# Optimization experiments

Measured on AMD Instinct MI355X. Metric: run time of the kernel, lower is better.

## Reference

```python
import jax, jax.numpy as jnp
import numpy as np
from jax.ops import segment_sum

NUM_HEADS = 16
NEG_INF = -jnp.inf


def setup_inputs() -> dict:
    key = jax.random.key(0)
    ks = jax.random.split(key, 12)
    D, H = 1024, NUM_HEADS
    SRC, TGT = 2048, 2048
    V, EV = 32000, 2000
    s = 1.0 / np.sqrt(D)
    return {
        "logits": jax.random.normal(ks[0], (TGT, V), jnp.float32),
        "extended_vocab_ids": jax.random.randint(ks[1], (SRC,), 0, V + EV, jnp.int32),
        "src_subtokens": jax.random.normal(ks[2], (SRC, D), jnp.float32),
        "tgt_subtokens": jax.random.normal(ks[3], (TGT, D), jnp.float32),
        "w_q": jax.random.normal(ks[4], (D, D), jnp.float32) * s,
        "b_q": jax.random.normal(ks[5], (D,), jnp.float32) * 0.02,
        "w_k": jax.random.normal(ks[6], (D, D), jnp.float32) * s,
        "b_k": jax.random.normal(ks[7], (D,), jnp.float32) * 0.02,
        "w_ptr": jax.random.normal(ks[8], (D,), jnp.float32) * s,
        "b_ptr": jax.random.normal(ks[9], (1,), jnp.float32) * 0.02,
        "len_vocab": V,
        "len_extended_vocab": EV,
    }


def _mha_attention(query, key, w_q, b_q, w_k, b_k):
    # SimpleMHA.unbatched_forward: project q/k, per-head scaled dot-product
    # softmax over src, mean over heads -> [TGT, SRC]
    TGT, D = query.shape
    SRC = key.shape[0]
    hd = D // NUM_HEADS
    q = (query @ w_q.T + b_q).reshape(TGT, NUM_HEADS, hd)
    k = (key @ w_k.T + b_k).reshape(SRC, NUM_HEADS, hd)
    scores = jnp.einsum("thd,shd->hts", q, k) / jnp.sqrt(jnp.float32(hd))
    attn = jax.nn.softmax(scores, axis=-1)  # [H, TGT, SRC]
    return attn.mean(axis=0)  # [TGT, SRC]


def reference(logits, extended_vocab_ids, src_subtokens, tgt_subtokens,
              w_q, b_q, w_k, b_k, w_ptr, b_ptr, len_vocab, len_extended_vocab):
    total = len_vocab + len_extended_vocab
    eps = jnp.finfo(jnp.float32).eps
    fmin = jnp.finfo(jnp.float32).min

    # copy gate: sigmoid(Linear(tgt)) -> [TGT, 1]
    copy_prob = jax.nn.sigmoid(tgt_subtokens @ w_ptr + b_ptr[0])[:, None]

    # attention distribution over src tokens [TGT, SRC]
    attn = _mha_attention(tgt_subtokens, src_subtokens, w_q, b_q, w_k, b_k)

    # attention @ one-hot(M) == scatter-add of attention columns by vocab id
    attn_vocab = segment_sum(attn.T, extended_vocab_ids, num_segments=total).T  # [TGT, total]
    attn_vocab = jnp.where(attn_vocab == 0, eps, attn_vocab)
    pointer_log_probs = jnp.log(attn_vocab)

    decoder_log_probs = jax.nn.log_softmax(logits, axis=1)
    decoder_log_probs = jnp.pad(decoder_log_probs, ((0, 0), (0, len_extended_vocab)),
                                constant_values=NEG_INF)

    p = jnp.stack([decoder_log_probs + jnp.log(1.0 - copy_prob),
                   pointer_log_probs + jnp.log(copy_prob)])
    p = jnp.where(p == NEG_INF, fmin, p)
    return jax.scipy.special.logsumexp(p, axis=0)
```

## Files before the change

### kernel.cpp

```cpp
#include <hip/hip_runtime.h>

typedef __attribute__((ext_vector_type(8))) short short8;
typedef __attribute__((ext_vector_type(4))) float f32x4;
typedef __attribute__((ext_vector_type(4))) unsigned int u32x4;
typedef unsigned short u16;
typedef unsigned int u32;

#define MFMA16 __builtin_amdgcn_mfma_f32_16x16x32_bf16

static constexpr int TGT = 2048, SRCN = 2048, DIM = 1024, NH = 16;
static constexpr int NV = 32000, NTOT = 34000;
#define FLT_EPS 1.1920928955078125e-07f

__device__ __forceinline__ u16 f2bf(float f) {
  unsigned u = __float_as_uint(f);
  return (u16)((u + 0x7FFFu + ((u >> 16) & 1u)) >> 16);
}

__device__ __forceinline__ int swz8(int row, int seg) {
  return row * 64 + ((seg ^ (row & 7)) << 3);
}

__global__ __launch_bounds__(256) void proj_gemm(
    const float* __restrict__ Xq, const float* __restrict__ Wq,
    const float* __restrict__ Bq, u16* __restrict__ Cq,
    const float* __restrict__ Xk, const float* __restrict__ Wk,
    const float* __restrict__ Bk, u16* __restrict__ Ck) {
  const int zz = blockIdx.z;
  const float* X = zz ? Xk : Xq;
  const float* W = zz ? Wk : Wq;
  const float* bias = zz ? Bk : Bq;
  u16* C = zz ? Ck : Cq;
  const float scale = zz ? 1.0f : 0.125f;

  __shared__ u16 As[128 * 32];
  __shared__ u16 Bs[128 * 32];
  const int n0 = blockIdx.x * 128, m0 = blockIdx.y * 128;
  const int tid = threadIdx.x, lane = tid & 63, w = tid >> 6;
  const int wr = w >> 1, wc = w & 1;
  const int srow = tid >> 1, shalf = tid & 1;
  f32x4 acc[4][4] = {};

  for (int k0 = 0; k0 < DIM; k0 += 32) {
    __syncthreads();
    {
      const float* pa = X + (size_t)(m0 + srow) * DIM + k0 + shalf * 16;
      const float* pb = W + (size_t)(n0 + srow) * DIM + k0 + shalf * 16;
      float4 a0 = ((const float4*)pa)[0], a1 = ((const float4*)pa)[1];
      float4 a2 = ((const float4*)pa)[2], a3 = ((const float4*)pa)[3];
      float4 b0 = ((const float4*)pb)[0], b1 = ((const float4*)pb)[1];
      float4 b2 = ((const float4*)pb)[2], b3 = ((const float4*)pb)[3];
      short8 wa0, wa1, wb0, wb1;
      wa0[0]=(short)f2bf(a0.x); wa0[1]=(short)f2bf(a0.y); wa0[2]=(short)f2bf(a0.z); wa0[3]=(short)f2bf(a0.w);
      wa0[4]=(short)f2bf(a1.x); wa0[5]=(short)f2bf(a1.y); wa0[6]=(short)f2bf(a1.z); wa0[7]=(short)f2bf(a1.w);
      wa1[0]=(short)f2bf(a2.x); wa1[1]=(short)f2bf(a2.y); wa1[2]=(short)f2bf(a2.z); wa1[3]=(short)f2bf(a2.w);
      wa1[4]=(short)f2bf(a3.x); wa1[5]=(short)f2bf(a3.y); wa1[6]=(short)f2bf(a3.z); wa1[7]=(short)f2bf(a3.w);
      wb0[0]=(short)f2bf(b0.x); wb0[1]=(short)f2bf(b0.y); wb0[2]=(short)f2bf(b0.z); wb0[3]=(short)f2bf(b0.w);
      wb0[4]=(short)f2bf(b1.x); wb0[5]=(short)f2bf(b1.y); wb0[6]=(short)f2bf(b1.z); wb0[7]=(short)f2bf(b1.w);
      wb1[0]=(short)f2bf(b2.x); wb1[1]=(short)f2bf(b2.y); wb1[2]=(short)f2bf(b2.z); wb1[3]=(short)f2bf(b2.w);
      wb1[4]=(short)f2bf(b3.x); wb1[5]=(short)f2bf(b3.y); wb1[6]=(short)f2bf(b3.z); wb1[7]=(short)f2bf(b3.w);
      int swz = (srow >> 1) & 3;
      int sg0 = ((shalf * 2 + 0) ^ swz) << 3;
      int sg1 = ((shalf * 2 + 1) ^ swz) << 3;
      *(short8*)&As[srow * 32 + sg0] = wa0;
      *(short8*)&As[srow * 32 + sg1] = wa1;
      *(short8*)&Bs[srow * 32 + sg0] = wb0;
      *(short8*)&Bs[srow * 32 + sg1] = wb1;
    }
    __syncthreads();
    const int kq = lane >> 4;
    short8 af[4], bfr[4];
    for (int f = 0; f < 4; ++f) {
      int ar = wr * 64 + f * 16 + (lane & 15);
      af[f] = *(const short8*)&As[ar * 32 + ((kq ^ ((ar >> 1) & 3)) << 3)];
      int br = wc * 64 + f * 16 + (lane & 15);
      bfr[f] = *(const short8*)&Bs[br * 32 + ((kq ^ ((br >> 1) & 3)) << 3)];
    }
    for (int fr = 0; fr < 4; ++fr)
      for (int fc = 0; fc < 4; ++fc)
        acc[fr][fc] = MFMA16(af[fr], bfr[fc], acc[fr][fc], 0, 0, 0);
  }

  for (int fc = 0; fc < 4; ++fc) {
    int col = n0 + wc * 64 + fc * 16 + (lane & 15);
    float bv = bias[col];
    for (int fr = 0; fr < 4; ++fr)
      for (int r = 0; r < 4; ++r) {
        int rowm = m0 + wr * 64 + fr * 16 + ((lane >> 4) << 2) + r;
        C[(size_t)rowm * DIM + col] = f2bf((acc[fr][fc][r] + bv) * scale);
      }
  }
}

__global__ __launch_bounds__(256) void zsum_kernel(const u16* __restrict__ Qb,
                                                   const u16* __restrict__ Kb,
                                                   float* __restrict__ Zinv) {
  __shared__ u16 Ks[64 * 64];
  const int h = blockIdx.x, t0 = blockIdx.y * 64;
  const int tid = threadIdx.x, lane = tid & 63, w = tid >> 6;
  const int arow = t0 + w * 16 + (lane & 15);
  const int acol = h * 64 + ((lane >> 4) << 3);
  short8 a0 = *(const short8*)&Qb[(size_t)arow * DIM + acol];
  short8 a1 = *(const short8*)&Qb[(size_t)arow * DIM + acol + 32];
  float zacc[4] = {0.f, 0.f, 0.f, 0.f};

  for (int s0 = 0; s0 < SRCN; s0 += 64) {
    __syncthreads();
    for (int q = tid; q < 512; q += 256) {
      int r = q >> 3, seg = q & 7;
      *(short8*)&Ks[swz8(r, seg)] = *(const short8*)&Kb[(size_t)(s0 + r) * DIM + h * 64 + seg * 8];
    }
    __syncthreads();
    for (int sub = 0; sub < 4; ++sub) {
      int brow = sub * 16 + (lane & 15);
      int slo = (lane >> 4);
      short8 b0 = *(const short8*)&Ks[swz8(brow, slo)];
      short8 b1 = *(const short8*)&Ks[swz8(brow, slo + 4)];
      f32x4 c = {0.f, 0.f, 0.f, 0.f};
      c = MFMA16(a0, b0, c, 0, 0, 0);
      c = MFMA16(a1, b1, c, 0, 0, 0);
      zacc[0] += __expf(c[0]); zacc[1] += __expf(c[1]);
      zacc[2] += __expf(c[2]); zacc[3] += __expf(c[3]);
    }
  }
  for (int d = 1; d < 16; d <<= 1) {
    zacc[0] += __shfl_xor(zacc[0], d, 64);
    zacc[1] += __shfl_xor(zacc[1], d, 64);
    zacc[2] += __shfl_xor(zacc[2], d, 64);
    zacc[3] += __shfl_xor(zacc[3], d, 64);
  }
  if ((lane & 15) == 0) {
    int trow = t0 + w * 16 + ((lane >> 4) << 2);
    for (int r = 0; r < 4; ++r)
      Zinv[h * TGT + trow + r] = 1.0f / (16.0f * zacc[r]);
  }
}

__global__ __launch_bounds__(256) void fused_mid_kernel(
    const u16* __restrict__ Qb, const u16* __restrict__ Kb,
    const float* __restrict__ Zinv, float* __restrict__ attn,
    const float* __restrict__ logits, const float* __restrict__ tgt,
    const float* __restrict__ w_ptr, const float* __restrict__ b_ptr,
    const int* __restrict__ ids, int* __restrict__ sperm,
    u32* __restrict__ segmap, float4* __restrict__ rowc) {
  __shared__ __align__(16) char smem[20480];
  const int b = blockIdx.x;
  const int tid = threadIdx.x, lane = tid & 63, w = tid >> 6;

  if (b == 0) {
    int* kk_ = (int*)smem;
    int* vv_ = (int*)(smem + 8192);
    for (int i = tid; i < 2048; i += 256) { kk_[i] = ids[i]; vv_[i] = i; }
    __syncthreads();
    for (int kk = 2; kk <= 2048; kk <<= 1)
      for (int j = kk >> 1; j > 0; j >>= 1) {
        for (int m = tid; m < 1024; m += 256) {
          int i = ((m & ~(j - 1)) << 1) | (m & (j - 1));
          int l = i | j;
          bool asc = ((i & kk) == 0);
          int ki = kk_[i], kl = kk_[l];
          if ((ki > kl) == asc) {
            kk_[i] = kl; kk_[l] = ki;
            int tv = vv_[i]; vv_[i] = vv_[l]; vv_[l] = tv;
          }
        }
        __syncthreads();
      }
    for (int i = tid; i < 2048; i += 256) sperm[i] = vv_[i];
    for (int i = tid; i < NTOT; i += 256) segmap[i] = 0xFFFFFFFFu;
    __syncthreads();
    for (int p = tid; p < 2048; p += 256) {
      int id = kk_[p];
      if (p > 0 && kk_[p - 1] == id) continue;
      int q = p + 1;
      while (q < 2048 && kk_[q] == id) ++q;
      segmap[id] = (u32)p | ((u32)(q - p) << 16);
    }
    return;
  }

  if (b <= 1024) {
    u16* Qs = (u16*)smem;
    u16* Ks = (u16*)(smem + 8192);
    float* izs = (float*)(smem + 16384);
    const int bb = b - 1;
    const int s0 = (bb & 31) * 64, t0 = (bb >> 5) * 64;
    const int wr = w >> 1, wc = w & 1;
    for (int q = tid; q < 1024; q += 256) izs[q] = Zinv[(q >> 6) * TGT + t0 + (q & 63)];
    f32x4 acc[2][2] = {};

    for (int h = 0; h < NH; ++h) {
      __syncthreads();
      for (int q = tid; q < 512; q += 256) {
        int r = q >> 3, seg = q & 7;
        *(short8*)&Qs[swz8(r, seg)] = *(const short8*)&Qb[(size_t)(t0 + r) * DIM + h * 64 + seg * 8];
        *(short8*)&Ks[swz8(r, seg)] = *(const short8*)&Kb[(size_t)(s0 + r) * DIM + h * 64 + seg * 8];
      }
      __syncthreads();
      f32x4 sc[2][2] = {};
      for (int kk = 0; kk < 2; ++kk) {
        int seg = (lane >> 4) + kk * 4;
        short8 a0 = *(const short8*)&Qs[swz8(wr * 32 + (lane & 15), seg)];
        short8 a1 = *(const short8*)&Qs[swz8(wr * 32 + 16 + (lane & 15), seg)];
        short8 b0 = *(const short8*)&Ks[swz8(wc * 32 + (lane & 15), seg)];
        short8 b1 = *(const short8*)&Ks[swz8(wc * 32 + 16 + (lane & 15), seg)];
        sc[0][0] = MFMA16(a0, b0, sc[0][0], 0, 0, 0);
        sc[0][1] = MFMA16(a0, b1, sc[0][1], 0, 0, 0);
        sc[1][0] = MFMA16(a1, b0, sc[1][0], 0, 0, 0);
        sc[1][1] = MFMA16(a1, b1, sc[1][1], 0, 0, 0);
      }
      for (int fr = 0; fr < 2; ++fr)
        for (int fc = 0; fc < 2; ++fc)
          for (int r = 0; r < 4; ++r) {
            float iz = izs[h * 64 + wr * 32 + fr * 16 + ((lane >> 4) << 2) + r];
            acc[fr][fc][r] += __expf(sc[fr][fc][r]) * iz;
          }
    }
    for (int fr = 0; fr < 2; ++fr)
      for (int fc = 0; fc < 2; ++fc)
        for (int r = 0; r < 4; ++r) {
          int t = t0 + wr * 32 + fr * 16 + ((lane >> 4) << 2) + r;
          int s = s0 + wc * 32 + fc * 16 + (lane & 15);
          attn[(size_t)t * SRCN + s] = acc[fr][fc][r];
        }
    return;
  }

  float* red = (float*)smem;
  const int t = b - 1025;
  const f32x4* l4 = (const f32x4*)(logits + (size_t)t * NV);
  float e0 = 0.f, e1 = 0.f, e2 = 0.f, e3 = 0.f;
  const f32x4 z4 = {0.f, 0.f, 0.f, 0.f};
#pragma unroll 2
  for (int pk = 0; pk < 8; ++pk) {
    int g0 = pk * 1024 + tid;
    int g1 = g0 + 256, g2 = g0 + 512, g3 = g0 + 768;
    bool d0 = g0 < NV / 4, d1 = g1 < NV / 4, d2 = g2 < NV / 4, d3 = g3 < NV / 4;
    f32x4 v0 = d0 ? l4[g0] : z4;
    f32x4 v1 = d1 ? l4[g1] : z4;
    f32x4 v2 = d2 ? l4[g2] : z4;
    f32x4 v3 = d3 ? l4[g3] : z4;
    float s0 = (__expf(v0.x) + __expf(v0.y)) + (__expf(v0.z) + __expf(v0.w));
    float s1 = (__expf(v1.x) + __expf(v1.y)) + (__expf(v1.z) + __expf(v1.w));
    float s2 = (__expf(v2.x) + __expf(v2.y)) + (__expf(v2.z) + __expf(v2.w));
    float s3 = (__expf(v3.x) + __expf(v3.y)) + (__expf(v3.z) + __expf(v3.w));
    e0 += d0 ? s0 : 0.f;
    e1 += d1 ? s1 : 0.f;
    e2 += d2 ? s2 : 0.f;
    e3 += d3 ? s3 : 0.f;
  }
  float es = (e0 + e1) + (e2 + e3);

  float4 xv = *(const float4*)&tgt[(size_t)t * DIM + tid * 4];
  float4 wv = *(const float4*)&w_ptr[tid * 4];
  float g = (xv.x * wv.x + xv.y * wv.y) + (xv.z * wv.z + xv.w * wv.w);
  for (int d = 1; d < 64; d <<= 1) {
    es += __shfl_xor(es, d, 64);
    g += __shfl_xor(g, d, 64);
  }
  if (lane == 0) { red[w] = es; red[4 + w] = g; }
  __syncthreads();
  if (tid == 0) {
    float tot = red[0] + red[1] + red[2] + red[3];
    float gs = red[4] + red[5] + red[6] + red[7] + b_ptr[0];
    float c = 1.0f / (1.0f + __expf(-gs));
    float4 rc;
    rc.x = (1.0f - c) / tot;
    rc.y = c * FLT_EPS;
    rc.z = c;
    rc.w = 0.f;
    rowc[t] = rc;
  }
}

__global__ __launch_bounds__(512) void out_kernel(
    const float* __restrict__ logits, const float4* __restrict__ rowc,
    const int* __restrict__ sperm, const u32* __restrict__ segmap,
    const float* __restrict__ attn, float* __restrict__ out) {
  const int t = blockIdx.x;
  const int tid = threadIdx.x;
  float4 rc = rowc[t];
  const float K1 = rc.x, Ceps = rc.y, cc = rc.z;
  const f32x4* l4 = (const f32x4*)(logits + (size_t)t * NV);
  const float* arow = attn + (size_t)t * SRCN;
  f32x4* o4 = (f32x4*)(out + (size_t)t * NTOT);
  const u32x4* m4 = (const u32x4*)segmap;

  auto psum = [&](u32 mv) -> float {
    if (mv == 0xFFFFFFFFu) return Ceps;
    int p = (int)(mv & 0xFFFFu), n = (int)(mv >> 16);
    float s = 0.f;
    for (int q = 0; q < n; ++q) s += arow[sperm[p + q]];
    return cc * s;
  };
  auto elem = [&](float v, bool d, u32 mv) -> float {
    float e = d ? __expf(v) : 0.f;
    return __logf(fmaf(e, K1, psum(mv)));
  };

  const f32x4 z4 = {0.f, 0.f, 0.f, 0.f};
#pragma unroll
  for (int pk = 0; pk < 4; ++pk) {
    int g0 = pk * 2048 + tid;
    int g1 = g0 + 512, g2 = g0 + 1024, g3 = g0 + 1536;
    u32x4 m0 = m4[g0], m1 = m4[g1], m2 = m4[g2], m3 = m4[g3];
    bool d0 = g0 < NV / 4, d1 = g1 < NV / 4, d2 = g2 < NV / 4, d3 = g3 < NV / 4;
    f32x4 v0 = d0 ? __builtin_nontemporal_load(&l4[g0]) : z4;
    f32x4 v1 = d1 ? __builtin_nontemporal_load(&l4[g1]) : z4;
    f32x4 v2 = d2 ? __builtin_nontemporal_load(&l4[g2]) : z4;
    f32x4 v3 = d3 ? __builtin_nontemporal_load(&l4[g3]) : z4;
    f32x4 o0, o1, o2, o3;
    o0.x = elem(v0.x, d0, m0.x); o0.y = elem(v0.y, d0, m0.y);
    o0.z = elem(v0.z, d0, m0.z); o0.w = elem(v0.w, d0, m0.w);
    o1.x = elem(v1.x, d1, m1.x); o1.y = elem(v1.y, d1, m1.y);
    o1.z = elem(v1.z, d1, m1.z); o1.w = elem(v1.w, d1, m1.w);
    o2.x = elem(v2.x, d2, m2.x); o2.y = elem(v2.y, d2, m2.y);
    o2.z = elem(v2.z, d2, m2.z); o2.w = elem(v2.w, d2, m2.w);
    o3.x = elem(v3.x, d3, m3.x); o3.y = elem(v3.y, d3, m3.y);
    o3.z = elem(v3.z, d3, m3.z); o3.w = elem(v3.w, d3, m3.w);
    __builtin_nontemporal_store(o0, &o4[g0]);
    __builtin_nontemporal_store(o1, &o4[g1]);
    __builtin_nontemporal_store(o2, &o4[g2]);
    __builtin_nontemporal_store(o3, &o4[g3]);
  }
  for (int g = 8192 + tid; g < NTOT / 4; g += 512) {
    u32x4 m = m4[g];
    f32x4 o;
    o.x = __logf(psum(m.x));
    o.y = __logf(psum(m.y));
    o.z = __logf(psum(m.z));
    o.w = __logf(psum(m.w));
    __builtin_nontemporal_store(o, &o4[g]);
  }
}

extern "C" void kernel_launch(void* const* d_in, const int* in_sizes, int n_in,
                              void* d_out, int out_size, void* d_ws, size_t ws_size,
                              hipStream_t stream) {
  const float* logits = (const float*)d_in[0];
  const int* ids      = (const int*)d_in[1];
  const float* src    = (const float*)d_in[2];
  const float* tgt    = (const float*)d_in[3];
  const float* w_q    = (const float*)d_in[4];
  const float* b_q    = (const float*)d_in[5];
  const float* w_k    = (const float*)d_in[6];
  const float* b_k    = (const float*)d_in[7];
  const float* w_ptr  = (const float*)d_in[8];
  const float* b_ptr  = (const float*)d_in[9];
  float* out = (float*)d_out;

  char* ws = (char*)d_ws;
  u16* Qb     = (u16*)(ws);
  u16* Kb     = (u16*)(ws + (size_t)4 * 1024 * 1024);
  float* Zinv = (float*)(ws + (size_t)8 * 1024 * 1024);
  float* attn = (float*)(ws + (size_t)8 * 1024 * 1024 + 131072);
  char* tail  = ws + (size_t)8 * 1024 * 1024 + 131072 + (size_t)16 * 1024 * 1024;
  int* sperm  = (int*)(tail);
  u32* segmap = (u32*)(tail + 8192);
  float4* rowc = (float4*)(tail + 8192 + 136000);

  proj_gemm<<<dim3(8, 16, 2), 256, 0, stream>>>(tgt, w_q, b_q, Qb, src, w_k, b_k, Kb);
  zsum_kernel<<<dim3(16, 32), 256, 0, stream>>>(Qb, Kb, Zinv);
  fused_mid_kernel<<<3073, 256, 0, stream>>>(Qb, Kb, Zinv, attn, logits, tgt,
                                             w_ptr, b_ptr, ids, sperm, segmap, rowc);
  out_kernel<<<TGT, 512, 0, stream>>>(logits, rowc, sperm, segmap, attn, out);
}
```

Measured before the change: 275.0 us.

## Rebalance independent row-stats and sort work across zsum and attention kernels

The independent work (logit softmax denominators, copy gate, id sort) is split across the two middle kernels. Half the row stats and the sort now run alongside the Z-sum kernel, the rest alongside the attention-column kernel, so the small zsum launch no longer underfills the GPU. The attention kernel also reads Zinv straight from global memory as float4 instead of staging it in shared memory. This balances load between launches, at the cost of more block-level branching.

Result: slower. 297.9 us (+8.4%).

```diff
diff --git a/kernel.cpp b/kernel.cpp
--- a/kernel.cpp
+++ b/kernel.cpp
@@ -19,6 +19,88 @@
 
 __device__ __forceinline__ int swz8(int row, int seg) {
   return row * 64 + ((seg ^ (row & 7)) << 3);
+}
+
+__device__ __forceinline__ void stats_row_body(
+    int t, const float* __restrict__ logits, const float* __restrict__ tgt,
+    const float* __restrict__ w_ptr, const float* __restrict__ b_ptr,
+    float4* __restrict__ rowc, int tid, int lane, int w, float* red) {
+  const f32x4* l4 = (const f32x4*)(logits + (size_t)t * NV);
+  float e0 = 0.f, e1 = 0.f, e2 = 0.f, e3 = 0.f;
+  const f32x4 z4 = {0.f, 0.f, 0.f, 0.f};
+#pragma unroll 2
+  for (int pk = 0; pk < 8; ++pk) {
+    int g0 = pk * 1024 + tid;
+    int g1 = g0 + 256, g2 = g0 + 512, g3 = g0 + 768;
+    bool d0 = g0 < NV / 4, d1 = g1 < NV / 4, d2 = g2 < NV / 4, d3 = g3 < NV / 4;
+    f32x4 v0 = d0 ? l4[g0] : z4;
+    f32x4 v1 = d1 ? l4[g1] : z4;
+    f32x4 v2 = d2 ? l4[g2] : z4;
+    f32x4 v3 = d3 ? l4[g3] : z4;
+    float s0 = (__expf(v0.x) + __expf(v0.y)) + (__expf(v0.z) + __expf(v0.w));
+    float s1 = (__expf(v1.x) + __expf(v1.y)) + (__expf(v1.z) + __expf(v1.w));
+    float s2 = (__expf(v2.x) + __expf(v2.y)) + (__expf(v2.z) + __expf(v2.w));
+    float s3 = (__expf(v3.x) + __expf(v3.y)) + (__expf(v3.z) + __expf(v3.w));
+    e0 += d0 ? s0 : 0.f;
+    e1 += d1 ? s1 : 0.f;
+    e2 += d2 ? s2 : 0.f;
+    e3 += d3 ? s3 : 0.f;
+  }
+  float es = (e0 + e1) + (e2 + e3);
+
+  float4 xv = *(const float4*)&tgt[(size_t)t * DIM + tid * 4];
+  float4 wv = *(const float4*)&w_ptr[tid * 4];
+  float g = (xv.x * wv.x + xv.y * wv.y) + (xv.z * wv.z + xv.w * wv.w);
+  for (int d = 1; d < 64; d <<= 1) {
+    es += __shfl_xor(es, d, 64);
+    g += __shfl_xor(g, d, 64);
+  }
+  if (lane == 0) { red[w] = es; red[4 + w] = g; }
+  __syncthreads();
+  if (tid == 0) {
+    float tot = red[0] + red[1] + red[2] + red[3];
+    float gs = red[4] + red[5] + red[6] + red[7] + b_ptr[0];
+    float c = 1.0f / (1.0f + __expf(-gs));
+    float4 rc;
+    rc.x = (1.0f - c) / tot;
+    rc.y = c * FLT_EPS;
+    rc.z = c;
+    rc.w = 0.f;
+    rowc[t] = rc;
+  }
+}
+
+__device__ __forceinline__ void sort_body(
+    const int* __restrict__ ids, int* __restrict__ sperm,
+    u32* __restrict__ segmap, int tid, char* smem) {
+  int* kk_ = (int*)smem;
+  int* vv_ = (int*)(smem + 8192);
+  for (int i = tid; i < 2048; i += 256) { kk_[i] = ids[i]; vv_[i] = i; }
+  __syncthreads();
+  for (int kk = 2; kk <= 2048; kk <<= 1)
+    for (int j = kk >> 1; j > 0; j >>= 1) {
+      for (int m = tid; m < 1024; m += 256) {
+        int i = ((m & ~(j - 1)) << 1) | (m & (j - 1));
+        int l = i | j;
+        bool asc = ((i & kk) == 0);
+        int ki = kk_[i], kl = kk_[l];
+        if ((ki > kl) == asc) {
+          kk_[i] = kl; kk_[l] = ki;
+          int tv = vv_[i]; vv_[i] = vv_[l]; vv_[l] = tv;
+        }
+      }
+      __syncthreads();
+    }
+  for (int i = tid; i < 2048; i += 256) sperm[i] = vv_[i];
+  for (int i = tid; i < NTOT; i += 256) segmap[i] = 0xFFFFFFFFu;
+  __syncthreads();
+  for (int p = tid; p < 2048; p += 256) {
+    int id = kk_[p];
+    if (p > 0 && kk_[p - 1] == id) continue;
+    int q = p + 1;
+    while (q < 2048 && kk_[q] == id) ++q;
+    segmap[id] = (u32)p | ((u32)(q - p) << 16);
+  }
 }
 
 __global__ __launch_bounds__(256) void proj_gemm(
@@ -92,185 +174,124 @@
   }
 }
 
-__global__ __launch_bounds__(256) void zsum_kernel(const u16* __restrict__ Qb,
-                                                   const u16* __restrict__ Kb,
-                                                   float* __restrict__ Zinv) {
-  __shared__ u16 Ks[64 * 64];
-  const int h = blockIdx.x, t0 = blockIdx.y * 64;
+__global__ __launch_bounds__(256) void fused_a_kernel(
+    const u16* __restrict__ Qb, const u16* __restrict__ Kb,
+    float* __restrict__ Zinv,
+    const float* __restrict__ logits, const float* __restrict__ tgt,
+    const float* __restrict__ w_ptr, const float* __restrict__ b_ptr,
+    const int* __restrict__ ids, int* __restrict__ sperm,
+    u32* __restrict__ segmap, float4* __restrict__ rowc) {
+  __shared__ __align__(16) char smem[16384];
+  const int b = blockIdx.x;
   const int tid = threadIdx.x, lane = tid & 63, w = tid >> 6;
-  const int arow = t0 + w * 16 + (lane & 15);
-  const int acol = h * 64 + ((lane >> 4) << 3);
-  short8 a0 = *(const short8*)&Qb[(size_t)arow * DIM + acol];
-  short8 a1 = *(const short8*)&Qb[(size_t)arow * DIM + acol + 32];
-  float zacc[4] = {0.f, 0.f, 0.f, 0.f};
-
-  for (int s0 = 0; s0 < SRCN; s0 += 64) {
-    __syncthreads();
-    for (int q = tid; q < 512; q += 256) {
-      int r = q >> 3, seg = q & 7;
-      *(short8*)&Ks[swz8(r, seg)] = *(const short8*)&Kb[(size_t)(s0 + r) * DIM + h * 64 + seg * 8];
-    }
-    __syncthreads();
-    for (int sub = 0; sub < 4; ++sub) {
-      int brow = sub * 16 + (lane & 15);
-      int slo = (lane >> 4);
-      short8 b0 = *(const short8*)&Ks[swz8(brow, slo)];
-      short8 b1 = *(const short8*)&Ks[swz8(brow, slo + 4)];
-      f32x4 c = {0.f, 0.f, 0.f, 0.f};
-      c = MFMA16(a0, b0, c, 0, 0, 0);
-      c = MFMA16(a1, b1, c, 0, 0, 0);
-      zacc[0] += __expf(c[0]); zacc[1] += __expf(c[1]);
-      zacc[2] += __expf(c[2]); zacc[3] += __expf(c[3]);
-    }
-  }
-  for (int d = 1; d < 16; d <<= 1) {
-    zacc[0] += __shfl_xor(zacc[0], d, 64);
-    zacc[1] += __shfl_xor(zacc[1], d, 64);
-    zacc[2] += __shfl_xor(zacc[2], d, 64);
-    zacc[3] += __shfl_xor(zacc[3], d, 64);
-  }
-  if ((lane & 15) == 0) {
-    int trow = t0 + w * 16 + ((lane >> 4) << 2);
-    for (int r = 0; r < 4; ++r)
-      Zinv[h * TGT + trow + r] = 1.0f / (16.0f * zacc[r]);
-  }
-}
-
-__global__ __launch_bounds__(256) void fused_mid_kernel(
+
+  if (b < 1024) {
+    stats_row_body(b, logits, tgt, w_ptr, b_ptr, rowc, tid, lane, w, (float*)smem);
+    return;
+  }
+  if (b == 1536) {
+    sort_body(ids, sperm, segmap, tid, smem);
+    return;
+  }
+  {
+    u16* Ks = (u16*)smem;
+    const int bb = b - 1024;
+    const int h = bb & 15, t0 = (bb >> 4) * 64;
+    const int arow = t0 + w * 16 + (lane & 15);
+    const int acol = h * 64 + ((lane >> 4) << 3);
+    short8 a0 = *(const short8*)&Qb[(size_t)arow * DIM + acol];
+    short8 a1 = *(const short8*)&Qb[(size_t)arow * DIM + acol + 32];
+    float zacc[4] = {0.f, 0.f, 0.f, 0.f};
+
+    for (int s0 = 0; s0 < SRCN; s0 += 64) {
+      __syncthreads();
+      for (int q = tid; q < 512; q += 256) {
+        int r = q >> 3, seg = q & 7;
+        *(short8*)&Ks[swz8(r, seg)] = *(const short8*)&Kb[(size_t)(s0 + r) * DIM + h * 64 + seg * 8];
+      }
+      __syncthreads();
+      for (int sub = 0; sub < 4; ++sub) {
+        int brow = sub * 16 + (lane & 15);
+        int slo = (lane >> 4);
+        short8 b0 = *(const short8*)&Ks[swz8(brow, slo)];
+        short8 b1 = *(const short8*)&Ks[swz8(brow, slo + 4)];
+        f32x4 c = {0.f, 0.f, 0.f, 0.f};
+        c = MFMA16(a0, b0, c, 0, 0, 0);
+        c = MFMA16(a1, b1, c, 0, 0, 0);
+        zacc[0] += __expf(c[0]); zacc[1] += __expf(c[1]);
+        zacc[2] += __expf(c[2]); zacc[3] += __expf(c[3]);
+      }
+    }
+    for (int d = 1; d < 16; d <<= 1) {
+      zacc[0] += __shfl_xor(zacc[0], d, 64);
+      zacc[1] += __shfl_xor(zacc[1], d, 64);
+      zacc[2] += __shfl_xor(zacc[2], d, 64);
+      zacc[3] += __shfl_xor(zacc[3], d, 64);
+    }
+    if ((lane & 15) == 0) {
+      int trow = t0 + w * 16 + ((lane >> 4) << 2);
+      for (int r = 0; r < 4; ++r)
+        Zinv[h * TGT + trow + r] = 1.0f / (16.0f * zacc[r]);
+    }
+  }
+}
+
+__global__ __launch_bounds__(256) void fused_b_kernel(
     const u16* __restrict__ Qb, const u16* __restrict__ Kb,
     const float* __restrict__ Zinv, float* __restrict__ attn,
     const float* __restrict__ logits, const float* __restrict__ tgt,
     const float* __restrict__ w_ptr, const float* __restrict__ b_ptr,
-    const int* __restrict__ ids, int* __restrict__ sperm,
-    u32* __restrict__ segmap, float4* __restrict__ rowc) {
-  __shared__ __align__(16) char smem[20480];
+    float4* __restrict__ rowc) {
+  __shared__ __align__(16) char smem[16384];
   const int b = blockIdx.x;
   const int tid = threadIdx.x, lane = tid & 63, w = tid >> 6;
 
-  if (b == 0) {
-    int* kk_ = (int*)smem;
-    int* vv_ = (int*)(smem + 8192);
-    for (int i = tid; i < 2048; i += 256) { kk_[i] = ids[i]; vv_[i] = i; }
+  if (b >= 1024) {
+    stats_row_body(b, logits, tgt, w_ptr, b_ptr, rowc, tid, lane, w, (float*)smem);
+    return;
+  }
+  u16* Qs = (u16*)smem;
+  u16* Ks = (u16*)(smem + 8192);
+  const int s0 = (b & 31) * 64, t0 = (b >> 5) * 64;
+  const int wr = w >> 1, wc = w & 1;
+  f32x4 acc[2][2] = {};
+
+  for (int h = 0; h < NH; ++h) {
     __syncthreads();
-    for (int kk = 2; kk <= 2048; kk <<= 1)
-      for (int j = kk >> 1; j > 0; j >>= 1) {
-        for (int m = tid; m < 1024; m += 256) {
-          int i = ((m & ~(j - 1)) << 1) | (m & (j - 1));
-          int l = i | j;
-          bool asc = ((i & kk) == 0);
-          int ki = kk_[i], kl = kk_[l];
-          if ((ki > kl) == asc) {
-            kk_[i] = kl; kk_[l] = ki;
-            int tv = vv_[i]; vv_[i] = vv_[l]; vv_[l] = tv;
-          }
-        }
-        __syncthreads();
-      }
-    for (int i = tid; i < 2048; i += 256) sperm[i] = vv_[i];
-    for (int i = tid; i < NTOT; i += 256) segmap[i] = 0xFFFFFFFFu;
+    for (int q = tid; q < 512; q += 256) {
+      int r = q >> 3, seg = q & 7;
+      *(short8*)&Qs[swz8(r, seg)] = *(const short8*)&Qb[(size_t)(t0 + r) * DIM + h * 64 + seg * 8];
+      *(short8*)&Ks[swz8(r, seg)] = *(const short8*)&Kb[(size_t)(s0 + r) * DIM + h * 64 + seg * 8];
+    }
     __syncthreads();
-    for (int p = tid; p < 2048; p += 256) {
-      int id = kk_[p];
-      if (p > 0 && kk_[p - 1] == id) continue;
-      int q = p + 1;
-      while (q < 2048 && kk_[q] == id) ++q;
-      segmap[id] = (u32)p | ((u32)(q - p) << 16);
-    }
-    return;
-  }
-
-  if (b <= 1024) {
-    u16* Qs = (u16*)smem;
-    u16* Ks = (u16*)(smem + 8192);
-    float* izs = (float*)(smem + 16384);
-    const int bb = b - 1;
-    const int s0 = (bb & 31) * 64, t0 = (bb >> 5) * 64;
-    const int wr = w >> 1, wc = w & 1;
-    for (int q = tid; q < 1024; q += 256) izs[q] = Zinv[(q >> 6) * TGT + t0 + (q & 63)];
-    f32x4 acc[2][2] = {};
-
-    for (int h = 0; h < NH; ++h) {
-      __syncthreads();
-      for (int q = tid; q < 512; q += 256) {
-        int r = q >> 3, seg = q & 7;
-        *(short8*)&Qs[swz8(r, seg)] = *(const short8*)&Qb[(size_t)(t0 + r) * DIM + h * 64 + seg * 8];
-        *(short8*)&Ks[swz8(r, seg)] = *(const short8*)&Kb[(size_t)(s0 + r) * DIM + h * 64 + seg * 8];
-      }
-      __syncthreads();
-      f32x4 sc[2][2] = {};
-      for (int kk = 0; kk < 2; ++kk) {
-        int seg = (lane >> 4) + kk * 4;
-        short8 a0 = *(const short8*)&Qs[swz8(wr * 32 + (lane & 15), seg)];
-        short8 a1 = *(const short8*)&Qs[swz8(wr * 32 + 16 + (lane & 15), seg)];
-        short8 b0 = *(const short8*)&Ks[swz8(wc * 32 + (lane & 15), seg)];
-        short8 b1 = *(const short8*)&Ks[swz8(wc * 32 + 16 + (lane & 15), seg)];
-        sc[0][0] = MFMA16(a0, b0, sc[0][0], 0, 0, 0);
-        sc[0][1] = MFMA16(a0, b1, sc[0][1], 0, 0, 0);
-        sc[1][0] = MFMA16(a1, b0, sc[1][0], 0, 0, 0);
-        sc[1][1] = MFMA16(a1, b1, sc[1][1], 0, 0, 0);
-      }
-      for (int fr = 0; fr < 2; ++fr)
-        for (int fc = 0; fc < 2; ++fc)
-          for (int r = 0; r < 4; ++r) {
-            float iz = izs[h * 64 + wr * 32 + fr * 16 + ((lane >> 4) << 2) + r];
-            acc[fr][fc][r] += __expf(sc[fr][fc][r]) * iz;
-          }
-    }
-    for (int fr = 0; fr < 2; ++fr)
+    f32x4 sc[2][2] = {};
+    for (int kk = 0; kk < 2; ++kk) {
+      int seg = (lane >> 4) + kk * 4;
+      short8 a0 = *(const short8*)&Qs[swz8(wr * 32 + (lane & 15), seg)];
+      short8 a1 = *(const short8*)&Qs[swz8(wr * 32 + 16 + (lane & 15), seg)];
+      short8 b0 = *(const short8*)&Ks[swz8(wc * 32 + (lane & 15), seg)];
+      short8 b1 = *(const short8*)&Ks[swz8(wc * 32 + 16 + (lane & 15), seg)];
+      sc[0][0] = MFMA16(a0, b0, sc[0][0], 0, 0, 0);
+      sc[0][1] = MFMA16(a0, b1, sc[0][1], 0, 0, 0);
+      sc[1][0] = MFMA16(a1, b0, sc[1][0], 0, 0, 0);
+      sc[1][1] = MFMA16(a1, b1, sc[1][1], 0, 0, 0);
+    }
+    for (int fr = 0; fr < 2; ++fr) {
+      int trow = t0 + wr * 32 + fr * 16 + ((lane >> 4) << 2);
+      float4 z4 = *(const float4*)&Zinv[h * TGT + trow];
+      float iz[4] = {z4.x, z4.y, z4.z, z4.w};
       for (int fc = 0; fc < 2; ++fc)
-        for (int r = 0; r < 4; ++r) {
-          int t = t0 + wr * 32 + fr * 16 + ((lane >> 4) << 2) + r;
-          int s = s0 + wc * 32 + fc * 16 + (lane & 15);
-          attn[(size_t)t * SRCN + s] = acc[fr][fc][r];
-        }
-    return;
-  }
-
-  float* red = (float*)smem;
-  const int t = b - 1025;
-  const f32x4* l4 = (const f32x4*)(logits + (size_t)t * NV);
-  float e0 = 0.f, e1 = 0.f, e2 = 0.f, e3 = 0.f;
-  const f32x4 z4 = {0.f, 0.f, 0.f, 0.f};
-#pragma unroll 2
-  for (int pk = 0; pk < 8; ++pk) {
-    int g0 = pk * 1024 + tid;
-    int g1 = g0 + 256, g2 = g0 + 512, g3 = g0 + 768;
-    bool d0 = g0 < NV / 4, d1 = g1 < NV / 4, d2 = g2 < NV / 4, d3 = g3 < NV / 4;
-    f32x4 v0 = d0 ? l4[g0] : z4;
-    f32x4 v1 = d1 ? l4[g1] : z4;
-    f32x4 v2 = d2 ? l4[g2] : z4;
-    f32x4 v3 = d3 ? l4[g3] : z4;
-    float s0 = (__expf(v0.x) + __expf(v0.y)) + (__expf(v0.z) + __expf(v0.w));
-    float s1 = (__expf(v1.x) + __expf(v1.y)) + (__expf(v1.z) + __expf(v1.w));
-    float s2 = (__expf(v2.x) + __expf(v2.y)) + (__expf(v2.z) + __expf(v2.w));
-    float s3 = (__expf(v3.x) + __expf(v3.y)) + (__expf(v3.z) + __expf(v3.w));
-    e0 += d0 ? s0 : 0.f;
-    e1 += d1 ? s1 : 0.f;
-    e2 += d2 ? s2 : 0.f;
-    e3 += d3 ? s3 : 0.f;
-  }
-  float es = (e0 + e1) + (e2 + e3);
-
-  float4 xv = *(const float4*)&tgt[(size_t)t * DIM + tid * 4];
-  float4 wv = *(const float4*)&w_ptr[tid * 4];
-  float g = (xv.x * wv.x + xv.y * wv.y) + (xv.z * wv.z + xv.w * wv.w);
-  for (int d = 1; d < 64; d <<= 1) {
-    es += __shfl_xor(es, d, 64);
-    g += __shfl_xor(g, d, 64);
-  }
-  if (lane == 0) { red[w] = es; red[4 + w] = g; }
-  __syncthreads();
-  if (tid == 0) {
-    float tot = red[0] + red[1] + red[2] + red[3];
-    float gs = red[4] + red[5] + red[6] + red[7] + b_ptr[0];
-    float c = 1.0f / (1.0f + __expf(-gs));
-    float4 rc;
-    rc.x = (1.0f - c) / tot;
-    rc.y = c * FLT_EPS;
-    rc.z = c;
-    rc.w = 0.f;
-    rowc[t] = rc;
-  }
+        for (int r = 0; r < 4; ++r)
+          acc[fr][fc][r] += __expf(sc[fr][fc][r]) * iz[r];
+    }
+  }
+  for (int fr = 0; fr < 2; ++fr)
+    for (int fc = 0; fc < 2; ++fc)
+      for (int r = 0; r < 4; ++r) {
+        int t = t0 + wr * 32 + fr * 16 + ((lane >> 4) << 2) + r;
+        int s = s0 + wc * 32 + fc * 16 + (lane & 15);
+        attn[(size_t)t * SRCN + s] = acc[fr][fc][r];
+      }
 }
 
 __global__ __launch_bounds__(512) void out_kernel(
@@ -360,8 +381,9 @@
   float4* rowc = (float4*)(tail + 8192 + 136000);
 
   proj_gemm<<<dim3(8, 16, 2), 256, 0, stream>>>(tgt, w_q, b_q, Qb, src, w_k, b_k, Kb);
-  zsum_kernel<<<dim3(16, 32), 256, 0, stream>>>(Qb, Kb, Zinv);
-  fused_mid_kernel<<<3073, 256, 0, stream>>>(Qb, Kb, Zinv, attn, logits, tgt,
-                                             w_ptr, b_ptr, ids, sperm, segmap, rowc);
+  fused_a_kernel<<<1537, 256, 0, stream>>>(Qb, Kb, Zinv, logits, tgt, w_ptr, b_ptr,
+                                           ids, sperm, segmap, rowc);
+  fused_b_kernel<<<2048, 256, 0, stream>>>(Qb, Kb, Zinv, attn, logits, tgt,
+                                           w_ptr, b_ptr, rowc);
   out_kernel<<<TGT, 512, 0, stream>>>(logits, rowc, sperm, segmap, attn, out);
 }
```

## Cache bf16 exp(logits) in stats pass and read it in output kernel

Applied to the files above, without the earlier changes.

The row-stats blocks now write exp(logits) as bf16 into a workspace buffer, and a new output kernel reads that buffer instead of re-reading fp32 logits and recomputing exp. This halves the logit read in the final pass but adds a 131MB bf16 write, and it lowers precision of the decoder term to bf16. Both output kernels now process rows in reverse order, apparently so the most recently written rows are still in cache. Zinv is also read straight from global memory instead of being staged in shared memory. The new path runs only if the workspace is large enough.

Result: slower. 327.0 us (+18.9%).

```diff
diff --git a/kernel.cpp b/kernel.cpp
--- a/kernel.cpp
+++ b/kernel.cpp
@@ -16,9 +16,103 @@
   unsigned u = __float_as_uint(f);
   return (u16)((u + 0x7FFFu + ((u >> 16) & 1u)) >> 16);
 }
+__device__ __forceinline__ float bf2f(u16 h) {
+  return __uint_as_float(((unsigned)h) << 16);
+}
 
 __device__ __forceinline__ int swz8(int row, int seg) {
   return row * 64 + ((seg ^ (row & 7)) << 3);
+}
+
+__device__ __forceinline__ void stats_row_body(
+    int t, const float* __restrict__ logits, const float* __restrict__ tgt,
+    const float* __restrict__ w_ptr, const float* __restrict__ b_ptr,
+    float4* __restrict__ rowc, u16* __restrict__ expb,
+    int tid, int lane, int w, float* red) {
+  const f32x4* l4 = (const f32x4*)(logits + (size_t)t * NV);
+  u16* erow = expb ? expb + (size_t)t * NV : (u16*)0;
+  float a0 = 0.f, a1 = 0.f, a2 = 0.f, a3 = 0.f;
+  const f32x4 z4 = {0.f, 0.f, 0.f, 0.f};
+#pragma unroll 2
+  for (int pk = 0; pk < 8; ++pk) {
+    int g0 = pk * 1024 + tid;
+    int g1 = g0 + 256, g2 = g0 + 512, g3 = g0 + 768;
+    bool d0 = g0 < NV / 4, d1 = g1 < NV / 4, d2 = g2 < NV / 4, d3 = g3 < NV / 4;
+    f32x4 v0 = d0 ? l4[g0] : z4;
+    f32x4 v1 = d1 ? l4[g1] : z4;
+    f32x4 v2 = d2 ? l4[g2] : z4;
+    f32x4 v3 = d3 ? l4[g3] : z4;
+    f32x4 e0, e1, e2, e3;
+    e0.x = __expf(v0.x); e0.y = __expf(v0.y); e0.z = __expf(v0.z); e0.w = __expf(v0.w);
+    e1.x = __expf(v1.x); e1.y = __expf(v1.y); e1.z = __expf(v1.z); e1.w = __expf(v1.w);
+    e2.x = __expf(v2.x); e2.y = __expf(v2.y); e2.z = __expf(v2.z); e2.w = __expf(v2.w);
+    e3.x = __expf(v3.x); e3.y = __expf(v3.y); e3.z = __expf(v3.z); e3.w = __expf(v3.w);
+    if (erow) {
+      if (d0) { ushort4 p = {f2bf(e0.x), f2bf(e0.y), f2bf(e0.z), f2bf(e0.w)}; *(ushort4*)&erow[g0 * 4] = p; }
+      if (d1) { ushort4 p = {f2bf(e1.x), f2bf(e1.y), f2bf(e1.z), f2bf(e1.w)}; *(ushort4*)&erow[g1 * 4] = p; }
+      if (d2) { ushort4 p = {f2bf(e2.x), f2bf(e2.y), f2bf(e2.z), f2bf(e2.w)}; *(ushort4*)&erow[g2 * 4] = p; }
+      if (d3) { ushort4 p = {f2bf(e3.x), f2bf(e3.y), f2bf(e3.z), f2bf(e3.w)}; *(ushort4*)&erow[g3 * 4] = p; }
+    }
+    a0 += d0 ? (e0.x + e0.y) + (e0.z + e0.w) : 0.f;
+    a1 += d1 ? (e1.x + e1.y) + (e1.z + e1.w) : 0.f;
+    a2 += d2 ? (e2.x + e2.y) + (e2.z + e2.w) : 0.f;
+    a3 += d3 ? (e3.x + e3.y) + (e3.z + e3.w) : 0.f;
+  }
+  float es = (a0 + a1) + (a2 + a3);
+
+  float4 xv = *(const float4*)&tgt[(size_t)t * DIM + tid * 4];
+  float4 wv = *(const float4*)&w_ptr[tid * 4];
+  float g = (xv.x * wv.x + xv.y * wv.y) + (xv.z * wv.z + xv.w * wv.w);
+  for (int d = 1; d < 64; d <<= 1) {
+    es += __shfl_xor(es, d, 64);
+    g += __shfl_xor(g, d, 64);
+  }
+  if (lane == 0) { red[w] = es; red[4 + w] = g; }
+  __syncthreads();
+  if (tid == 0) {
+    float tot = red[0] + red[1] + red[2] + red[3];
+    float gs = red[4] + red[5] + red[6] + red[7] + b_ptr[0];
+    float c = 1.0f / (1.0f + __expf(-gs));
+    float4 rc;
+    rc.x = (1.0f - c) / tot;
+    rc.y = c * FLT_EPS;
+    rc.z = c;
+    rc.w = 0.f;
+    rowc[t] = rc;
+  }
+}
+
+__device__ __forceinline__ void sort_body(
+    const int* __restrict__ ids, int* __restrict__ sperm,
+    u32* __restrict__ segmap, int tid, char* smem) {
+  int* kk_ = (int*)smem;
+  int* vv_ = (int*)(smem + 8192);
+  for (int i = tid; i < 2048; i += 256) { kk_[i] = ids[i]; vv_[i] = i; }
+  __syncthreads();
+  for (int kk = 2; kk <= 2048; kk <<= 1)
+    for (int j = kk >> 1; j > 0; j >>= 1) {
+      for (int m = tid; m < 1024; m += 256) {
+        int i = ((m & ~(j - 1)) << 1) | (m & (j - 1));
+        int l = i | j;
+        bool asc = ((i & kk) == 0);
+        int ki = kk_[i], kl = kk_[l];
+        if ((ki > kl) == asc) {
+          kk_[i] = kl; kk_[l] = ki;
+          int tv = vv_[i]; vv_[i] = vv_[l]; vv_[l] = tv;
+        }
+      }
+      __syncthreads();
+    }
+  for (int i = tid; i < 2048; i += 256) sperm[i] = vv_[i];
+  for (int i = tid; i < NTOT; i += 256) segmap[i] = 0xFFFFFFFFu;
+  __syncthreads();
+  for (int p = tid; p < 2048; p += 256) {
+    int id = kk_[p];
+    if (p > 0 && kk_[p - 1] == id) continue;
+    int q = p + 1;
+    while (q < 2048 && kk_[q] == id) ++q;
+    segmap[id] = (u32)p | ((u32)(q - p) << 16);
+  }
 }
 
 __global__ __launch_bounds__(256) void proj_gemm(
@@ -142,134 +236,128 @@
     const float* __restrict__ logits, const float* __restrict__ tgt,
     const float* __restrict__ w_ptr, const float* __restrict__ b_ptr,
     const int* __restrict__ ids, int* __restrict__ sperm,
-    u32* __restrict__ segmap, float4* __restrict__ rowc) {
-  __shared__ __align__(16) char smem[20480];
+    u32* __restrict__ segmap, float4* __restrict__ rowc,
+    u16* __restrict__ expb) {
+  __shared__ __align__(16) char smem[16384];
   const int b = blockIdx.x;
   const int tid = threadIdx.x, lane = tid & 63, w = tid >> 6;
 
   if (b == 0) {
-    int* kk_ = (int*)smem;
-    int* vv_ = (int*)(smem + 8192);
-    for (int i = tid; i < 2048; i += 256) { kk_[i] = ids[i]; vv_[i] = i; }
-    __syncthreads();
-    for (int kk = 2; kk <= 2048; kk <<= 1)
-      for (int j = kk >> 1; j > 0; j >>= 1) {
-        for (int m = tid; m < 1024; m += 256) {
-          int i = ((m & ~(j - 1)) << 1) | (m & (j - 1));
-          int l = i | j;
-          bool asc = ((i & kk) == 0);
-          int ki = kk_[i], kl = kk_[l];
-          if ((ki > kl) == asc) {
-            kk_[i] = kl; kk_[l] = ki;
-            int tv = vv_[i]; vv_[i] = vv_[l]; vv_[l] = tv;
-          }
-        }
-        __syncthreads();
+    sort_body(ids, sperm, segmap, tid, smem);
+    return;
+  }
+  if (b > 1024) {
+    stats_row_body(b - 1025, logits, tgt, w_ptr, b_ptr, rowc, expb,
+                   tid, lane, w, (float*)smem);
+    return;
+  }
+  u16* Qs = (u16*)smem;
+  u16* Ks = (u16*)(smem + 8192);
+  const int bb = b - 1;
+  const int s0 = (bb & 31) * 64, t0 = (bb >> 5) * 64;
+  const int wr = w >> 1, wc = w & 1;
+  f32x4 acc[2][2] = {};
+
+  for (int h = 0; h < NH; ++h) {
+    __syncthreads();
+    for (int q = tid; q < 512; q += 256) {
+      int r = q >> 3, seg = q & 7;
+      *(short8*)&Qs[swz8(r, seg)] = *(const short8*)&Qb[(size_t)(t0 + r) * DIM + h * 64 + seg * 8];
+      *(short8*)&Ks[swz8(r, seg)] = *(const short8*)&Kb[(size_t)(s0 + r) * DIM + h * 64 + seg * 8];
+    }
+    __syncthreads();
+    f32x4 sc[2][2] = {};
+    for (int kk = 0; kk < 2; ++kk) {
+      int seg = (lane >> 4) + kk * 4;
+      short8 a0 = *(const short8*)&Qs[swz8(wr * 32 + (lane & 15), seg)];
+      short8 a1 = *(const short8*)&Qs[swz8(wr * 32 + 16 + (lane & 15), seg)];
+      short8 b0 = *(const short8*)&Ks[swz8(wc * 32 + (lane & 15), seg)];
+      short8 b1 = *(const short8*)&Ks[swz8(wc * 32 + 16 + (lane & 15), seg)];
+      sc[0][0] = MFMA16(a0, b0, sc[0][0], 0, 0, 0);
+      sc[0][1] = MFMA16(a0, b1, sc[0][1], 0, 0, 0);
+      sc[1][0] = MFMA16(a1, b0, sc[1][0], 0, 0, 0);
+      sc[1][1] = MFMA16(a1, b1, sc[1][1], 0, 0, 0);
+    }
+    for (int fr = 0; fr < 2; ++fr) {
+      int trow = t0 + wr * 32 + fr * 16 + ((lane >> 4) << 2);
+      float4 z4 = *(const float4*)&Zinv[h * TGT + trow];
+      float iz[4] = {z4.x, z4.y, z4.z, z4.w};
+      for (int fc = 0; fc < 2; ++fc)
+        for (int r = 0; r < 4; ++r)
+          acc[fr][fc][r] += __expf(sc[fr][fc][r]) * iz[r];
+    }
+  }
+  for (int fr = 0; fr < 2; ++fr)
+    for (int fc = 0; fc < 2; ++fc)
+      for (int r = 0; r < 4; ++r) {
+        int t = t0 + wr * 32 + fr * 16 + ((lane >> 4) << 2) + r;
+        int s = s0 + wc * 32 + fc * 16 + (lane & 15);
+        attn[(size_t)t * SRCN + s] = acc[fr][fc][r];
       }
-    for (int i = tid; i < 2048; i += 256) sperm[i] = vv_[i];
-    for (int i = tid; i < NTOT; i += 256) segmap[i] = 0xFFFFFFFFu;
-    __syncthreads();
-    for (int p = tid; p < 2048; p += 256) {
-      int id = kk_[p];
-      if (p > 0 && kk_[p - 1] == id) continue;
-      int q = p + 1;
-      while (q < 2048 && kk_[q] == id) ++q;
-      segmap[id] = (u32)p | ((u32)(q - p) << 16);
-    }
-    return;
-  }
-
-  if (b <= 1024) {
-    u16* Qs = (u16*)smem;
-    u16* Ks = (u16*)(smem + 8192);
-    float* izs = (float*)(smem + 16384);
-    const int bb = b - 1;
-    const int s0 = (bb & 31) * 64, t0 = (bb >> 5) * 64;
-    const int wr = w >> 1, wc = w & 1;
-    for (int q = tid; q < 1024; q += 256) izs[q] = Zinv[(q >> 6) * TGT + t0 + (q & 63)];
-    f32x4 acc[2][2] = {};
-
-    for (int h = 0; h < NH; ++h) {
-      __syncthreads();
-      for (int q = tid; q < 512; q += 256) {
-        int r = q >> 3, seg = q & 7;
-        *(short8*)&Qs[swz8(r, seg)] = *(const short8*)&Qb[(size_t)(t0 + r) * DIM + h * 64 + seg * 8];
-        *(short8*)&Ks[swz8(r, seg)] = *(const short8*)&Kb[(size_t)(s0 + r) * DIM + h * 64 + seg * 8];
-      }
-      __syncthreads();
-      f32x4 sc[2][2] = {};
-      for (int kk = 0; kk < 2; ++kk) {
-        int seg = (lane >> 4) + kk * 4;
-        short8 a0 = *(const short8*)&Qs[swz8(wr * 32 + (lane & 15), seg)];
-        short8 a1 = *(const short8*)&Qs[swz8(wr * 32 + 16 + (lane & 15), seg)];
-        short8 b0 = *(const short8*)&Ks[swz8(wc * 32 + (lane & 15), seg)];
-        short8 b1 = *(const short8*)&Ks[swz8(wc * 32 + 16 + (lane & 15), seg)];
-        sc[0][0] = MFMA16(a0, b0, sc[0][0], 0, 0, 0);
-        sc[0][1] = MFMA16(a0, b1, sc[0][1], 0, 0, 0);
-        sc[1][0] = MFMA16(a1, b0, sc[1][0], 0, 0, 0);
-        sc[1][1] = MFMA16(a1, b1, sc[1][1], 0, 0, 0);
-      }
-      for (int fr = 0; fr < 2; ++fr)
-        for (int fc = 0; fc < 2; ++fc)
-          for (int r = 0; r < 4; ++r) {
-            float iz = izs[h * 64 + wr * 32 + fr * 16 + ((lane >> 4) << 2) + r];
-            acc[fr][fc][r] += __expf(sc[fr][fc][r]) * iz;
-          }
-    }
-    for (int fr = 0; fr < 2; ++fr)
-      for (int fc = 0; fc < 2; ++fc)
-        for (int r = 0; r < 4; ++r) {
-          int t = t0 + wr * 32 + fr * 16 + ((lane >> 4) << 2) + r;
-          int s = s0 + wc * 32 + fc * 16 + (lane & 15);
-          attn[(size_t)t * SRCN + s] = acc[fr][fc][r];
-        }
-    return;
-  }
-
-  float* red = (float*)smem;
-  const int t = b - 1025;
-  const f32x4* l4 = (const f32x4*)(logits + (size_t)t * NV);
-  float e0 = 0.f, e1 = 0.f, e2 = 0.f, e3 = 0.f;
-  const f32x4 z4 = {0.f, 0.f, 0.f, 0.f};
-#pragma unroll 2
-  for (int pk = 0; pk < 8; ++pk) {
-    int g0 = pk * 1024 + tid;
-    int g1 = g0 + 256, g2 = g0 + 512, g3 = g0 + 768;
+}
+
+__global__ __launch_bounds__(512) void out_expb_kernel(
+    const u16* __restrict__ expb, const float4* __restrict__ rowc,
+    const int* __restrict__ sperm, const u32* __restrict__ segmap,
+    const float* __restrict__ attn, float* __restrict__ out) {
+  const int t = (TGT - 1) - blockIdx.x;
+  const int tid = threadIdx.x;
+  float4 rc = rowc[t];
+  const float K1 = rc.x, Ceps = rc.y, cc = rc.z;
+  const ushort4* e4 = (const ushort4*)(expb + (size_t)t * NV);
+  const float* arow = attn + (size_t)t * SRCN;
+  f32x4* o4 = (f32x4*)(out + (size_t)t * NTOT);
+  const u32x4* m4 = (const u32x4*)segmap;
+
+  auto psum = [&](u32 mv) -> float {
+    if (mv == 0xFFFFFFFFu) return Ceps;
+    int p = (int)(mv & 0xFFFFu), n = (int)(mv >> 16);
+    float s = 0.f;
+    for (int q = 0; q < n; ++q) s += arow[sperm[p + q]];
+    return cc * s;
+  };
+
+  const ushort4 hz = {0, 0, 0, 0};
+#pragma unroll
+  for (int pk = 0; pk < 4; ++pk) {
+    int g0 = pk * 2048 + tid;
+    int g1 = g0 + 512, g2 = g0 + 1024, g3 = g0 + 1536;
+    u32x4 m0 = m4[g0], m1 = m4[g1], m2 = m4[g2], m3 = m4[g3];
     bool d0 = g0 < NV / 4, d1 = g1 < NV / 4, d2 = g2 < NV / 4, d3 = g3 < NV / 4;
-    f32x4 v0 = d0 ? l4[g0] : z4;
-    f32x4 v1 = d1 ? l4[g1] : z4;
-    f32x4 v2 = d2 ? l4[g2] : z4;
-    f32x4 v3 = d3 ? l4[g3] : z4;
-    float s0 = (__expf(v0.x) + __expf(v0.y)) + (__expf(v0.z) + __expf(v0.w));
-    float s1 = (__expf(v1.x) + __expf(v1.y)) + (__expf(v1.z) + __expf(v1.w));
-    float s2 = (__expf(v2.x) + __expf(v2.y)) + (__expf(v2.z) + __expf(v2.w));
-    float s3 = (__expf(v3.x) + __expf(v3.y)) + (__expf(v3.z) + __expf(v3.w));
-    e0 += d0 ? s0 : 0.f;
-    e1 += d1 ? s1 : 0.f;
-    e2 += d2 ? s2 : 0.f;
-    e3 += d3 ? s3 : 0.f;
-  }
-  float es = (e0 + e1) + (e2 + e3);
-
-  float4 xv = *(const float4*)&tgt[(size_t)t * DIM + tid * 4];
-  float4 wv = *(const float4*)&w_ptr[tid * 4];
-  float g = (xv.x * wv.x + xv.y * wv.y) + (xv.z * wv.z + xv.w * wv.w);
-  for (int d = 1; d < 64; d <<= 1) {
-    es += __shfl_xor(es, d, 64);
-    g += __shfl_xor(g, d, 64);
-  }
-  if (lane == 0) { red[w] = es; red[4 + w] = g; }
-  __syncthreads();
-  if (tid == 0) {
-    float tot = red[0] + red[1] + red[2] + red[3];
-    float gs = red[4] + red[5] + red[6] + red[7] + b_ptr[0];
-    float c = 1.0f / (1.0f + __expf(-gs));
-    float4 rc;
-    rc.x = (1.0f - c) / tot;
-    rc.y = c * FLT_EPS;
-    rc.z = c;
-    rc.w = 0.f;
-    rowc[t] = rc;
+    ushort4 h0 = d0 ? e4[g0] : hz;
+    ushort4 h1 = d1 ? e4[g1] : hz;
+    ushort4 h2 = d2 ? e4[g2] : hz;
+    ushort4 h3 = d3 ? e4[g3] : hz;
+    f32x4 o0, o1, o2, o3;
+    o0.x = __logf(fmaf(bf2f(h0.x), K1, psum(m0.x)));
+    o0.y = __logf(fmaf(bf2f(h0.y), K1, psum(m0.y)));
+    o0.z = __logf(fmaf(bf2f(h0.z), K1, psum(m0.z)));
+    o0.w = __logf(fmaf(bf2f(h0.w), K1, psum(m0.w)));
+    o1.x = __logf(fmaf(bf2f(h1.x), K1, psum(m1.x)));
+    o1.y = __logf(fmaf(bf2f(h1.y), K1, psum(m1.y)));
+    o1.z = __logf(fmaf(bf2f(h1.z), K1, psum(m1.z)));
+    o1.w = __logf(fmaf(bf2f(h1.w), K1, psum(m1.w)));
+    o2.x = __logf(fmaf(bf2f(h2.x), K1, psum(m2.x)));
+    o2.y = __logf(fmaf(bf2f(h2.y), K1, psum(m2.y)));
+    o2.z = __logf(fmaf(bf2f(h2.z), K1, psum(m2.z)));
+    o2.w = __logf(fmaf(bf2f(h2.w), K1, psum(m2.w)));
+    o3.x = __logf(fmaf(bf2f(h3.x), K1, psum(m3.x)));
+    o3.y = __logf(fmaf(bf2f(h3.y), K1, psum(m3.y)));
+    o3.z = __logf(fmaf(bf2f(h3.z), K1, psum(m3.z)));
+    o3.w = __logf(fmaf(bf2f(h3.w), K1, psum(m3.w)));
+    __builtin_nontemporal_store(o0, &o4[g0]);
+    __builtin_nontemporal_store(o1, &o4[g1]);
+    __builtin_nontemporal_store(o2, &o4[g2]);
+    __builtin_nontemporal_store(o3, &o4[g3]);
+  }
+  for (int g = 8192 + tid; g < NTOT / 4; g += 512) {
+    u32x4 m = m4[g];
+    f32x4 o;
+    o.x = __logf(psum(m.x));
+    o.y = __logf(psum(m.y));
+    o.z = __logf(psum(m.z));
+    o.w = __logf(psum(m.w));
+    __builtin_nontemporal_store(o, &o4[g]);
   }
 }
 
@@ -277,7 +365,7 @@
     const float* __restrict__ logits, const float4* __restrict__ rowc,
     const int* __restrict__ sperm, const u32* __restrict__ segmap,
     const float* __restrict__ attn, float* __restrict__ out) {
-  const int t = blockIdx.x;
+  const int t = (TGT - 1) - blockIdx.x;
   const int tid = threadIdx.x;
   float4 rc = rowc[t];
   const float K1 = rc.x, Ceps = rc.y, cc = rc.z;
@@ -354,14 +442,22 @@
   u16* Kb     = (u16*)(ws + (size_t)4 * 1024 * 1024);
   float* Zinv = (float*)(ws + (size_t)8 * 1024 * 1024);
   float* attn = (float*)(ws + (size_t)8 * 1024 * 1024 + 131072);
-  char* tail  = ws + (size_t)8 * 1024 * 1024 + 131072 + (size_t)16 * 1024 * 1024;
-  int* sperm  = (int*)(tail);
-  u32* segmap = (u32*)(tail + 8192);
-  float4* rowc = (float4*)(tail + 8192 + 136000);
+  size_t tail_off = (size_t)8 * 1024 * 1024 + 131072 + (size_t)16 * 1024 * 1024;
+  int* sperm  = (int*)(ws + tail_off);
+  u32* segmap = (u32*)(ws + tail_off + 8192);
+  float4* rowc = (float4*)(ws + tail_off + 8192 + 136000);
+  size_t expb_off = (tail_off + 8192 + 136000 + 32768 + 255) & ~(size_t)255;
+  size_t expb_bytes = (size_t)TGT * NV * 2;
+  bool use_expb = ws_size >= expb_off + expb_bytes;
+  u16* expb = use_expb ? (u16*)(ws + expb_off) : (u16*)0;
 
   proj_gemm<<<dim3(8, 16, 2), 256, 0, stream>>>(tgt, w_q, b_q, Qb, src, w_k, b_k, Kb);
   zsum_kernel<<<dim3(16, 32), 256, 0, stream>>>(Qb, Kb, Zinv);
   fused_mid_kernel<<<3073, 256, 0, stream>>>(Qb, Kb, Zinv, attn, logits, tgt,
-                                             w_ptr, b_ptr, ids, sperm, segmap, rowc);
-  out_kernel<<<TGT, 512, 0, stream>>>(logits, rowc, sperm, segmap, attn, out);
-}
+                                             w_ptr, b_ptr, ids, sperm, segmap,
+                                             rowc, expb);
+  if (use_expb)
+    out_expb_kernel<<<TGT, 512, 0, stream>>>(expb, rowc, sperm, segmap, attn, out);
+  else
+    out_kernel<<<TGT, 512, 0, stream>>>(logits, rowc, sperm, segmap, attn, out);
+}
```
